# Optimization experiments

Measured on AMD Instinct MI355X. Metric: run time of the kernel, lower is better.

Reference implementation:

```python
import jax, jax.numpy as jnp
import numpy as np

B, T_ENC, T_DEC = 64, 512, 400
IN_DIM, R = 80, 2
D_ENC, D_ATT, D_PRE = 256, 256, 128
NEG_INF = -1e9


def _gru(x, h, Wi, Wh, bi, bh):
    # PyTorch GRUCell math
    gi = x @ Wi + bi
    gh = h @ Wh + bh
    ir, iz, inn = jnp.split(gi, 3, axis=-1)
    hr, hz, hn = jnp.split(gh, 3, axis=-1)
    r = jax.nn.sigmoid(ir + hr)
    z = jax.nn.sigmoid(iz + hz)
    n = jnp.tanh(inn + r * hn)
    return (1.0 - z) * n + z * h


def setup_inputs() -> dict:
    key = jax.random.key(0)
    ks = jax.random.split(key, 32)
    s = 0.05
    d_in = IN_DIM * R
    inp = {
        "encoder_outputs": jax.random.normal(ks[0], (B, T_ENC, D_ENC), jnp.float32),
        "inputs": jax.random.normal(ks[1], (B, T_DEC, d_in), jnp.float32),
        "memory_lengths": jax.random.randint(ks[2], (B,), T_ENC // 2, T_ENC + 1).astype(jnp.int32),
        # prenet
        "pre_W1": s * jax.random.normal(ks[3], (d_in, 256), jnp.float32),
        "pre_b1": jnp.zeros((256,), jnp.float32),
        "pre_W2": s * jax.random.normal(ks[4], (256, 128), jnp.float32),
        "pre_b2": jnp.zeros((128,), jnp.float32),
        # Bahdanau attention
        "mem_W": s * jax.random.normal(ks[5], (D_ENC, D_ATT), jnp.float32),
        "q_W": s * jax.random.normal(ks[6], (256, D_ATT), jnp.float32),
        "v_W": s * jax.random.normal(ks[7], (D_ATT, 1), jnp.float32),
        # attention GRUCell: input = cat(prenet 128, attention 256) = 384
        "att_Wi": s * jax.random.normal(ks[8], (384, 768), jnp.float32),
        "att_Wh": s * jax.random.normal(ks[9], (256, 768), jnp.float32),
        "att_bi": jnp.zeros((768,), jnp.float32),
        "att_bh": jnp.zeros((768,), jnp.float32),
        # project_to_decoder_in
        "proj_in_W": s * jax.random.normal(ks[10], (512, 256), jnp.float32),
        "proj_in_b": jnp.zeros((256,), jnp.float32),
        # decoder GRUCells
        "dec1_Wi": s * jax.random.normal(ks[11], (256, 768), jnp.float32),
        "dec1_Wh": s * jax.random.normal(ks[12], (256, 768), jnp.float32),
        "dec1_bi": jnp.zeros((768,), jnp.float32),
        "dec1_bh": jnp.zeros((768,), jnp.float32),
        "dec2_Wi": s * jax.random.normal(ks[13], (256, 768), jnp.float32),
        "dec2_Wh": s * jax.random.normal(ks[14], (256, 768), jnp.float32),
        "dec2_bi": jnp.zeros((768,), jnp.float32),
        "dec2_bh": jnp.zeros((768,), jnp.float32),
        # output projections
        "mel_W": s * jax.random.normal(ks[15], (256, d_in), jnp.float32),
        "mel_b": jnp.zeros((d_in,), jnp.float32),
        "gate_W": s * jax.random.normal(ks[16], (256, R), jnp.float32),
        "gate_b": jnp.zeros((R,), jnp.float32),
    }
    return inp


def _decoder_forward(encoder_outputs, inputs, memory_lengths,
                     pre_W1, pre_b1, pre_W2, pre_b2,
                     mem_W, q_W, v_W,
                     att_Wi, att_Wh, att_bi, att_bh,
                     proj_in_W, proj_in_b,
                     dec1_Wi, dec1_Wh, dec1_bi, dec1_bh,
                     dec2_Wi, dec2_Wh, dec2_bi, dec2_bh,
                     mel_W, mel_b, gate_W, gate_b):
    Bq, Tq, _ = encoder_outputs.shape
    processed_memory = encoder_outputs @ mem_W  # (B, T_enc, D_att)
    valid = jnp.arange(Tq)[None, :] < memory_lengths[:, None]  # (B, T_enc)

    # teacher forcing: input at step t is inputs[t-1], zeros at t=0
    prev = jnp.concatenate([jnp.zeros_like(inputs[:, :1]), inputs[:, :-1]], axis=1)
    prev = jnp.swapaxes(prev, 0, 1)  # (T_dec, B, in_dim*r)

    def prenet(x):
        # dropout is identity in eval mode
        h = jax.nn.relu(x @ pre_W1 + pre_b1)
        return jax.nn.relu(h @ pre_W2 + pre_b2)

    def step(carry, x_prev):
        att_h, h1, h2, cur_att = carry
        pre = prenet(x_prev)  # (B, 128)
        cell_in = jnp.concatenate([pre, cur_att], axis=-1)  # (B, 384)
        att_h = _gru(cell_in, att_h, att_Wi, att_Wh, att_bi, att_bh)  # (B, 256)
        # Bahdanau alignment over encoder memory
        score = jnp.squeeze(
            jnp.tanh(processed_memory + (att_h @ q_W)[:, None, :]) @ v_W, -1)  # (B, T_enc)
        score = jnp.where(valid, score, NEG_INF)
        align = jax.nn.softmax(score, axis=-1)
        cur_att = jnp.einsum('bt,btd->bd', align, encoder_outputs)  # (B, 256)
        dec_in = jnp.concatenate([att_h, cur_att], axis=-1) @ proj_in_W + proj_in_b
        h1 = _gru(dec_in, h1, dec1_Wi, dec1_Wh, dec1_bi, dec1_bh)
        d = h1 + dec_in
        h2 = _gru(d, h2, dec2_Wi, dec2_Wh, dec2_bi, dec2_bh)
        d = h2 + d
        gate = jax.nn.sigmoid(d @ gate_W + gate_b)  # (B, r)
        out = d @ mel_W + mel_b  # (B, in_dim*r)
        return (att_h, h1, h2, cur_att), (out, align, gate)

    z = jnp.zeros((Bq, 256), encoder_outputs.dtype)
    init = (z, z, z, z)
    _, (outs, aligns, gates) = jax.lax.scan(step, init, prev)
    outputs = jnp.swapaxes(outs, 0, 1)      # (B, T_dec, in_dim*r)
    alignments = jnp.swapaxes(aligns, 0, 1)  # (B, T_dec, T_enc)
    gates = jnp.swapaxes(gates, 0, 1)        # (B, T_dec, r)
    return outputs, alignments, gates


def reference(encoder_outputs, inputs, memory_lengths,
              pre_W1, pre_b1, pre_W2, pre_b2,
              mem_W, q_W, v_W,
              att_Wi, att_Wh, att_bi, att_bh,
              proj_in_W, proj_in_b,
              dec1_Wi, dec1_Wh, dec1_bi, dec1_bh,
              dec2_Wi, dec2_Wh, dec2_bi, dec2_bh,
              mel_W, mel_b, gate_W, gate_b):
    return _decoder_forward(encoder_outputs, inputs, memory_lengths,
                            pre_W1, pre_b1, pre_W2, pre_b2,
                            mem_W, q_W, v_W,
                            att_Wi, att_Wh, att_bi, att_bh,
                            proj_in_W, proj_in_b,
                            dec1_Wi, dec1_Wh, dec1_bi, dec1_bh,
                            dec2_Wi, dec2_Wh, dec2_bi, dec2_bh,
                            mel_W, mel_b, gate_W, gate_b)
```

## Files before the change

### kernel.cpp

```cpp
#include <hip/hip_runtime.h>

#define TDEC 400
#define NTH 512
#define NWG 256

typedef float f32x4 __attribute__((ext_vector_type(4)));
typedef unsigned u32x4 __attribute__((ext_vector_type(4)));
typedef unsigned u32x2 __attribute__((ext_vector_type(2)));

#define OFF_BAR   0
#define OFF_ATTH  11264
#define OFF_H1    44032
#define OFF_H2    76800
#define OFF_CURP  109568
#define OFF_ATTS  125952
#define OFF_Q     126208
#define ZERO_FLOATS 142592
#define OFF_D1    142592
#define OFF_SUMS  158976
#define OFF_C1    184576
#define OFF_PRE   185600
#define OFF_PMB   1824000
#define OFF_ENCB  6018304
#define OFF_D2A   10212608
#define T_WIT_A   10212608
#define T_WHT_A   10507520
#define T_M1T     10704128
#define T_WHT1    11097344
#define T_PJT     11293952
#define T_WIT2    11425024
#define T_WHT2    11621632
#define T_QWT     11818240
#define T_M1      11883776
#define OFF_BLOB  16766208

#define BLOB_N   26112
#define BLOB_STR 26624
#define BO_AI  0
#define BO_AH  4608
#define BO_Q   7680
#define BO_M1  8704
#define BO_H1  14848
#define BO_PJ  17920
#define BO_I2  19968
#define BO_H2  23040

#define AOFF 4096000
#define GOFF 17203200

#define MSTI  (8*1024)
#define GENI  (9*1024)
#define FAILI (10*1024)

__device__ __forceinline__ float fsig(float x){ return 1.0f/(1.0f+__expf(-x)); }
__device__ __forceinline__ float ftanh(float x){ float e = __expf(2.0f*x); return 1.0f - 2.0f/(e+1.0f); }
__device__ __forceinline__ float blo(unsigned u){ return __uint_as_float(u<<16); }
__device__ __forceinline__ float bhi(unsigned u){ return __uint_as_float(u & 0xffff0000u); }

__device__ __forceinline__ f32x4 cload16(const float* p){
  f32x4 r;
  asm volatile("global_load_dwordx4 %0, %1, off sc0 sc1" : "=v"(r) : "v"(p));
  return r;
}
__device__ __forceinline__ f32x4 cload16w(const float* p){
  f32x4 r;
  asm volatile("global_load_dwordx4 %0, %1, off sc0 sc1\n\ts_waitcnt vmcnt(0)" : "=v"(r) : "v"(p));
  return r;
}
__device__ __forceinline__ u32x4 cload16u(const unsigned short* p){
  u32x4 r;
  asm volatile("global_load_dwordx4 %0, %1, off sc0 sc1" : "=v"(r) : "v"(p));
  return r;
}
__device__ __forceinline__ float aload4(const float* p){
  unsigned u = __hip_atomic_load((const unsigned*)p, __ATOMIC_RELAXED, __HIP_MEMORY_SCOPE_AGENT);
  return __uint_as_float(u);
}
__device__ __forceinline__ void astore4(float* p, float v){
  __hip_atomic_store((unsigned*)p, __float_as_uint(v), __ATOMIC_RELAXED, __HIP_MEMORY_SCOPE_AGENT);
}
__device__ __forceinline__ void aadd(float* p, float v){
  __hip_atomic_fetch_add(p, v, __ATOMIC_RELAXED, __HIP_MEMORY_SCOPE_AGENT);
}
__device__ __forceinline__ int aloadi(const int* p){
  return __hip_atomic_load(p, __ATOMIC_RELAXED, __HIP_MEMORY_SCOPE_AGENT);
}

__device__ __forceinline__ void ldsbar(){
  __builtin_amdgcn_sched_barrier(0);
  asm volatile("s_waitcnt lgkmcnt(0)" ::: "memory");
  __builtin_amdgcn_s_barrier();
  __builtin_amdgcn_sched_barrier(0);
}

__device__ __forceinline__ void gbar(int* bar, int g, int l, int n){
  asm volatile("s_waitcnt vmcnt(0)" ::: "memory");
  __syncthreads();
  if (threadIdx.x == 0){
    if (aloadi(&bar[FAILI]) == 0){
      int a = __hip_atomic_fetch_add(&bar[(l&7)*1024 + g*64], 1, __ATOMIC_RELAXED, __HIP_MEMORY_SCOPE_AGENT);
      if (a == 8*n - 1){
        int m = __hip_atomic_fetch_add(&bar[MSTI + g*64], 1, __ATOMIC_RELAXED, __HIP_MEMORY_SCOPE_AGENT);
        if (m == 8*n - 1)
          __hip_atomic_store(&bar[GENI + g*64], n, __ATOMIC_RELAXED, __HIP_MEMORY_SCOPE_AGENT);
      }
      int sp = 0;
      while (aloadi(&bar[GENI + g*64]) < n){
        __builtin_amdgcn_s_sleep(1);
        if (++sp > (1<<20)){
          __hip_atomic_store(&bar[FAILI], 1, __ATOMIC_RELAXED, __HIP_MEMORY_SCOPE_AGENT);
          break;
        }
      }
    }
  }
  __syncthreads();
}

__device__ __forceinline__ unsigned short f2bf(float f){
  unsigned u = __float_as_uint(f);
  return (unsigned short)((u + 0x7fffu + ((u>>16)&1u)) >> 16);
}

template<int N8>
__device__ __forceinline__ float bdot(const unsigned short* wr, const float* xr){
  f32x4 accA = 0.f, accB = 0.f;
  #pragma unroll 4
  for (int k = 0; k < N8; ++k){
    u32x4 u = *(const u32x4*)(wr + k*8);
    f32x4 a = *(const f32x4*)(xr + k*8);
    f32x4 b = *(const f32x4*)(xr + k*8 + 4);
    f32x4 w0, w1;
    w0[0]=blo(u[0]); w0[1]=bhi(u[0]); w0[2]=blo(u[1]); w0[3]=bhi(u[1]);
    w1[0]=blo(u[2]); w1[1]=bhi(u[2]); w1[2]=blo(u[3]); w1[3]=bhi(u[3]);
    accA += w0*a; accB += w1*b;
  }
  f32x4 s = accA + accB;
  return s[0]+s[1]+s[2]+s[3];
}

__global__ __launch_bounds__(256, 1) void transpose_k(const float* __restrict__ in,
                                                      float* __restrict__ outp, int K, int C){
  __shared__ float tl[32][33];
  int c0 = blockIdx.x * 32, k0 = blockIdx.y * 32;
  int tx = threadIdx.x & 31, ty = threadIdx.x >> 5;
  for (int i = ty; i < 32; i += 8){
    int k = k0 + i, c = c0 + tx;
    if (k < K && c < C) tl[i][tx] = in[k * C + c];
  }
  __syncthreads();
  for (int i = ty; i < 32; i += 8){
    int c = c0 + i, k = k0 + tx;
    if (c < C && k < K) outp[c * K + k] = tl[tx][i];
  }
}

__global__ __launch_bounds__(128, 1) void fuse_k(const float* __restrict__ projW,
    const float* __restrict__ d1Wi, float* __restrict__ M1){
  int jt = blockIdx.x % 6, i = blockIdx.x / 6;
  int j = jt * 128 + threadIdx.x;
  float acc = 0.f;
  for (int k = 0; k < 256; ++k) acc += projW[i*256+k] * d1Wi[k*768+j];
  M1[i*768+j] = acc;
}

__global__ __launch_bounds__(256, 1) void c1_k(const float* __restrict__ projB,
    const float* __restrict__ d1Wi, const float* __restrict__ d1Bi, float* __restrict__ C1){
  int j = blockIdx.x * 256 + threadIdx.x;
  float acc = d1Bi[j];
  for (int k = 0; k < 256; ++k) acc += projB[k] * d1Wi[k*768+j];
  C1[j] = acc;
}

__global__ __launch_bounds__(512, 1) void pack_k(float* __restrict__ ws){
  int sl = blockIdx.x;
  const float* TAI = ws + T_WIT_A;
  const float* TAH = ws + T_WHT_A;
  const float* TM1 = ws + T_M1T;
  const float* TH1 = ws + T_WHT1;
  const float* TPJ = ws + T_PJT;
  const float* TI2 = ws + T_WIT2;
  const float* TH2 = ws + T_WHT2;
  const float* TQ  = ws + T_QWT;
  unsigned short* blob = (unsigned short*)(ws + OFF_BLOB) + (size_t)sl * BLOB_STR;
  for (int idx = threadIdx.x; idx < BLOB_N; idx += 512){
    float v; int cs, k, o;
    if (idx < BO_AH){ cs = idx / 384; k = idx - cs*384;
      v = TAI[((cs%3)*256 + sl*4 + cs/3)*384 + k]; }
    else if (idx < BO_Q){ o = idx - BO_AH; cs = o >> 8; k = o & 255;
      v = TAH[((cs%3)*256 + sl*4 + cs/3)*256 + k]; }
    else if (idx < BO_M1){ o = idx - BO_Q; cs = o >> 8; k = o & 255;
      v = TQ[(sl*4 + cs)*256 + k]; }
    else if (idx < BO_H1){ o = idx - BO_M1; cs = o >> 9; k = o & 511;
      v = TM1[((cs%3)*256 + sl*4 + cs/3)*512 + k]; }
    else if (idx < BO_PJ){ o = idx - BO_H1; cs = o >> 8; k = o & 255;
      v = TH1[((cs%3)*256 + sl*4 + cs/3)*256 + k]; }
    else if (idx < BO_I2){ o = idx - BO_PJ; cs = o >> 9; k = o & 511;
      v = TPJ[(sl*4 + cs)*512 + k]; }
    else if (idx < BO_H2){ o = idx - BO_I2; cs = o >> 8; k = o & 255;
      v = TI2[((cs%3)*256 + sl*4 + cs/3)*256 + k]; }
    else { o = idx - BO_H2; cs = o >> 8; k = o & 255;
      v = TH2[((cs%3)*256 + sl*4 + cs/3)*256 + k]; }
    blob[idx] = f2bf(v);
  }
}

__global__ __launch_bounds__(256, 1) void qt_k(const float* __restrict__ ws,
                                               float* __restrict__ out){
  unsigned short* qtb = (unsigned short*)(out + GOFF);
  const float* TQ = ws + T_QWT;
  int idx = blockIdx.x * 256 + threadIdx.x;
  int it = idx >> 11, j = (idx >> 3) & 255, e = idx & 7;
  qtb[idx] = f2bf(TQ[j*256 + it*8 + e]);
}

__global__ __launch_bounds__(NTH, 1) void prenet_k(float* __restrict__ ws,
    const float* __restrict__ inp, const float* __restrict__ W1, const float* __restrict__ B1,
    const float* __restrict__ W2, const float* __restrict__ B2){
  __shared__ float xT[160 * 33];
  __shared__ float hT[256 * 33];
  int t = blockIdx.x, half = blockIdx.y, tid = threadIdx.x;
  int bbase = half * 32;
  for (int r = tid; r < 32 * 160; r += NTH){
    int b2 = r / 160; int k = r - b2 * 160;
    xT[k * 33 + b2] = (t == 0) ? 0.f : inp[((bbase + b2) * TDEC + (t - 1)) * 160 + k];
  }
  __syncthreads();
  int bl = tid & 31, slot = tid >> 5;
  float acc1[16];
  #pragma unroll
  for (int i = 0; i < 16; ++i) acc1[i] = 0.f;
  for (int k = 0; k < 160; ++k){
    float xv = xT[k * 33 + bl];
    const float* wr = W1 + k * 256 + slot * 16;
    #pragma unroll
    for (int i = 0; i < 16; ++i) acc1[i] += xv * wr[i];
  }
  #pragma unroll
  for (int i = 0; i < 16; ++i){
    int c = slot * 16 + i;
    hT[c * 33 + bl] = fmaxf(acc1[i] + B1[c], 0.f);
  }
  __syncthreads();
  float acc2[8];
  #pragma unroll
  for (int i = 0; i < 8; ++i) acc2[i] = 0.f;
  for (int k = 0; k < 256; ++k){
    float hv = hT[k * 33 + bl];
    const float* wr = W2 + k * 128 + slot * 8;
    #pragma unroll
    for (int i = 0; i < 8; ++i) acc2[i] += hv * wr[i];
  }
  unsigned short* dst = (unsigned short*)(ws + OFF_PRE) + (size_t)t*8192 + (bbase + bl)*128 + slot*8;
  u32x4 pk;
  #pragma unroll
  for (int i = 0; i < 4; ++i){
    float v0 = fmaxf(acc2[2*i] + B2[slot*8 + 2*i], 0.f);
    float v1 = fmaxf(acc2[2*i+1] + B2[slot*8 + 2*i+1], 0.f);
    pk[i] = (unsigned)f2bf(v0) | ((unsigned)f2bf(v1) << 16);
  }
  *(u32x4*)dst = pk;
}

__global__ __launch_bounds__(NTH, 1) void pm_k(float* __restrict__ ws,
    const float* __restrict__ enc, const float* __restrict__ memW){
  int wg = blockIdx.x, tid = threadIdx.x;
  int b = wg & 63, th = wg >> 6;
  int slot = tid & 7, tt = tid >> 3;
  int trow = th * 64 + tt;
  const float* er = enc + ((size_t)(b * 512 + trow)) * 256;
  f32x4 acc[8];
  #pragma unroll
  for (int i = 0; i < 8; ++i) acc[i] = 0.f;
  for (int k = 0; k < 256; ++k){
    float ev = er[k];
    const f32x4* wr = (const f32x4*)(memW + k * 256 + slot * 32);
    #pragma unroll
    for (int i = 0; i < 8; ++i) acc[i] += ev * wr[i];
  }
  unsigned short* pmB = (unsigned short*)(ws + OFF_PMB);
  unsigned short* dst = pmB + ((size_t)(b * 512 + trow)) * 256 + slot * 32;
  #pragma unroll
  for (int i = 0; i < 8; ++i){
    u32x2 pk;
    pk[0] = (unsigned)f2bf(acc[i][0]) | ((unsigned)f2bf(acc[i][1]) << 16);
    pk[1] = (unsigned)f2bf(acc[i][2]) | ((unsigned)f2bf(acc[i][3]) << 16);
    *(u32x2*)(dst + i * 4) = pk;
  }
  const float* e2 = enc + ((size_t)(b * 512 + th * 64)) * 256;
  unsigned* eb = (unsigned*)((unsigned short*)(ws + OFF_ENCB) + ((size_t)(b * 512 + th * 64)) * 256);
  for (int i = tid; i < 64 * 128; i += NTH){
    float v0 = e2[i * 2], v1 = e2[i * 2 + 1];
    eb[i] = (unsigned)f2bf(v0) | ((unsigned)f2bf(v1) << 16);
  }
}

__global__ __launch_bounds__(NTH, 2) void decoder_k(
    float* __restrict__ ws, float* __restrict__ out,
    const int* __restrict__ memlen,
    const float* __restrict__ vW,
    const float* __restrict__ attBi, const float* __restrict__ attBh,
    const float* __restrict__ projB,
    const float* __restrict__ d1Bh,
    const float* __restrict__ d2Bi, const float* __restrict__ d2Bh)
{
  const int wg = blockIdx.x, tid = threadIdx.x;
  int* bar = (int*)ws;
  float* attH = ws + OFF_ATTH;
  float* h1a  = ws + OFF_H1;
  float* h2a  = ws + OFF_H2;
  float* const curB[2]  = { ws + OFF_CURP, ws + OFF_Q };
  float* const attSB[2] = { ws + OFF_ATTS, ws + OFF_ATTS + 64 };
  float* d1v  = ws + OFF_D1;
  const float* C1v = ws + OFF_C1;
  const unsigned short* preB16 = (const unsigned short*)(ws + OFF_PRE);
  const unsigned short* pmB  = (const unsigned short*)(ws + OFF_PMB);
  const unsigned short* encB = (const unsigned short*)(ws + OFF_ENCB);
  const unsigned short* qtb = (const unsigned short*)(out + GOFF);
  float* d2a  = ws + OFF_D2A;

  __shared__ float BUF[12416];
  __shared__ float qL[256], vL[256];
  __shared__ float eL[128];
  __shared__ float ewGi[192], ewGh[192], pdec[128];

  if (tid < 256) vL[tid] = vW[tid];

  const int g = wg >> 6, l = wg & 63;
  const int sl = l;
  const int b0 = g << 4;
  const int b2 = b0 + (l >> 2), ch2 = l & 3;
  const int len2 = memlen[b2];
  const unsigned short* blob = (const unsigned short*)(ws + OFF_BLOB) + (size_t)sl * BLOB_STR;

  const int bq = tid & 15, x = tid >> 4;
  const int cs = (x >= 12) ? (x - 12) : x;
  const int gg = cs % 3, jh = cs / 3;
  const int col = gg * 256 + sl * 4 + jh;

  const int r0 = tid >> 6, c0 = (tid & 63) << 2;
  const int r1 = r0 + 8;
  const int prr = tid >> 4, pcc = (tid & 15) * 8;

  u32x4 pmv[8], env[8];
  {
    int te = tid >> 2, part = tid & 3;
    const u32x4* pmp = (const u32x4*)(pmB + ((size_t)(b2*512 + ch2*128 + te))*256 + part*64);
    #pragma unroll
    for (int i = 0; i < 8; ++i) pmv[i] = pmp[i];
    int ich = tid >> 5, dblk = tid & 31;
    const unsigned short* ep = encB + ((size_t)(b2*512 + ch2*128 + ich*8))*256 + dblk*8;
    #pragma unroll
    for (int i = 0; i < 8; ++i) env[i] = *(const u32x4*)(ep + i*256);
  }

  f32x4 pH0, pH1, pC0, pC1;
  float pS0, pS1;
  u32x4 ppre = 0u;
  {
    const float* gHn = attH + 16384 + b0*256;
    const float* gCn = curB[1] + b0*256;
    pH0 = cload16(gHn + (r0<<8) + c0); pH1 = cload16(gHn + (r1<<8) + c0);
    pC0 = cload16(gCn + (r0<<8) + c0); pC1 = cload16(gCn + (r1<<8) + c0);
    pS0 = aload4(attSB[1] + b0 + r0);  pS1 = aload4(attSB[1] + b0 + r1);
    if (tid < 256) ppre = cload16u(preB16 + (b0 + prr)*128 + pcc);
  }

  int bn = 0;
  for (int t = 0; t < TDEC; ++t){
    const int w = t & 1, rb = w ^ 1;
    f32x4 eA0, eA1, eH0, eH1, eG0, eG1;

    {
      float* xL = BUF;
      float* hL = BUF + 6208;
      asm volatile("s_waitcnt vmcnt(0)" : "+v"(pH0),"+v"(pH1),"+v"(pC0),"+v"(pC1),"+v"(ppre));
      float iv0 = pS0 > 0.f ? 1.f/pS0 : 0.f, iv1 = pS1 > 0.f ? 1.f/pS1 : 0.f;
      if (tid < 256){
        float* xd = xL + prr*388 + pcc;
        xd[0]=blo(ppre[0]); xd[1]=bhi(ppre[0]); xd[2]=blo(ppre[1]); xd[3]=bhi(ppre[1]);
        xd[4]=blo(ppre[2]); xd[5]=bhi(ppre[2]); xd[6]=blo(ppre[3]); xd[7]=bhi(ppre[3]);
      }
      *(f32x4*)(hL + r0*260 + c0) = pH0; *(f32x4*)(hL + r1*260 + c0) = pH1;
      *(f32x4*)(xL + r0*388 + 128 + c0) = pC0*iv0; *(f32x4*)(xL + r1*388 + 128 + c0) = pC1*iv1;
      if (tid < 64) astore4(curB[w] + wg*64 + tid, 0.f);
      if (sl == 0 && tid < 16) astore4(attSB[w] + b0 + tid, 0.f);
      ldsbar();
      if (x < 12)
        ewGi[cs*16 + bq] = bdot<48>(blob + BO_AI + cs*384, xL + bq*388) + attBi[col];
      else if (x < 24)
        ewGh[cs*16 + bq] = bdot<32>(blob + BO_AH + cs*256, hL + bq*260) + attBh[col];
      ldsbar();
      if (tid < 64){
        int bt = tid & 15, jj = tid >> 4;
        int j = sl*4 + jj;
        float ir = ewGi[(jj*3+0)*16+bt] + ewGh[(jj*3+0)*16+bt];
        float iz = ewGi[(jj*3+1)*16+bt] + ewGh[(jj*3+1)*16+bt];
        float inn = ewGi[(jj*3+2)*16+bt];
        float hn  = ewGh[(jj*3+2)*16+bt];
        float rg = fsig(ir), z = fsig(iz);
        float n = ftanh(inn + rg * hn);
        float h = hL[bt*260 + j];
        astore4(attH + w*16384 + (b0+bt)*256 + j, (1.f - z)*n + z*h);
      }
    }
    gbar(bar, g, l, ++bn);

    {
      float* ctxP = BUF;
      float* qIn  = BUF + 8192;
      eA0 = cload16(attH + w*16384 + ((b0+r0)<<8) + c0);
      eA1 = cload16(attH + w*16384 + ((b0+r1)<<8) + c0);
      eH0 = cload16(h1a + rb*16384 + ((b0+r0)<<8) + c0);
      eH1 = cload16(h1a + rb*16384 + ((b0+r1)<<8) + c0);
      eG0 = cload16(h2a + rb*16384 + ((b0+r0)<<8) + c0);
      eG1 = cload16(h2a + rb*16384 + ((b0+r1)<<8) + c0);
      if (tid < 64){
        f32x4 v = cload16w(attH + w*16384 + b2*256 + tid*4);
        *(f32x4*)(qIn + tid*4) = v;
      }
      ldsbar();
      {
        int lane = tid & 63;
        int j = (tid >> 6)*32 + (lane & 31), hf = lane >> 5;
        const unsigned short* qw = qtb + j*8 + (size_t)hf*32768;
        const float* qx = qIn + hf*128;
        f32x4 aA = 0.f, aB = 0.f;
        #pragma unroll 4
        for (int it = 0; it < 16; ++it){
          u32x4 u = *(const u32x4*)(qw + (size_t)it*2048);
          f32x4 a = *(const f32x4*)(qx + it*8);
          f32x4 b = *(const f32x4*)(qx + it*8 + 4);
          f32x4 w0, w1;
          w0[0]=blo(u[0]); w0[1]=bhi(u[0]); w0[2]=blo(u[1]); w0[3]=bhi(u[1]);
          w1[0]=blo(u[2]); w1[1]=bhi(u[2]); w1[2]=blo(u[3]); w1[3]=bhi(u[3]);
          aA += w0*a; aB += w1*b;
        }
        f32x4 s4 = aA + aB;
        float s = s4[0]+s4[1]+s4[2]+s4[3];
        s += __shfl_xor(s, 32);
        if (hf == 0) qL[j] = s;
      }
      ldsbar();
      {
        int te = tid >> 2, part = tid & 3;
        int ge = ch2*128 + te;
        float a4 = 0.f;
        #pragma unroll
        for (int i = 0; i < 8; ++i){
          u32x4 u = pmv[i];
          int kb = part*64 + i*8;
          a4 += ftanh(blo(u[0]) + qL[kb+0]) * vL[kb+0];
          a4 += ftanh(bhi(u[0]) + qL[kb+1]) * vL[kb+1];
          a4 += ftanh(blo(u[1]) + qL[kb+2]) * vL[kb+2];
          a4 += ftanh(bhi(u[1]) + qL[kb+3]) * vL[kb+3];
          a4 += ftanh(blo(u[2]) + qL[kb+4]) * vL[kb+4];
          a4 += ftanh(bhi(u[2]) + qL[kb+5]) * vL[kb+5];
          a4 += ftanh(blo(u[3]) + qL[kb+6]) * vL[kb+6];
          a4 += ftanh(bhi(u[3]) + qL[kb+7]) * vL[kb+7];
        }
        a4 += __shfl_xor(a4, 1);
        a4 += __shfl_xor(a4, 2);
        float e = (ge < len2) ? __expf(a4) : 0.f;
        if (part == 0){
          eL[te] = e;
          out[AOFF + ((size_t)(b2*TDEC + t))*512 + ge] = e;
        }
      }
      ldsbar();
      if (tid < 64){
        float s = eL[tid] + eL[tid + 64];
        #pragma unroll
        for (int o = 32; o > 0; o >>= 1) s += __shfl_down(s, o);
        if (tid == 0) aadd(attSB[w] + b2, s);
      }
      {
        int ich = tid >> 5, dblk = tid & 31;
        f32x4 acA = 0.f, acB = 0.f;
        #pragma unroll
        for (int i = 0; i < 8; ++i){
          u32x4 u = env[i];
          float e = eL[ich*8 + i];
          acA[0] += e*blo(u[0]); acA[1] += e*bhi(u[0]);
          acA[2] += e*blo(u[1]); acA[3] += e*bhi(u[1]);
          acB[0] += e*blo(u[2]); acB[1] += e*bhi(u[2]);
          acB[2] += e*blo(u[3]); acB[3] += e*bhi(u[3]);
        }
        *(f32x4*)(ctxP + tid*8) = acA;
        *(f32x4*)(ctxP + tid*8 + 4) = acB;
      }
      ldsbar();
      if (tid < 256){
        int dblk = tid >> 3, d = tid & 7;
        float s = 0.f;
        #pragma unroll
        for (int i = 0; i < 16; ++i) s += ctxP[i*256 + dblk*8 + d];
        aadd(curB[w] + b2*256 + dblk*8 + d, s);
      }
    }
    gbar(bar, g, l, ++bn);

    {
      float* yL  = BUF;
      float* h1L = BUF + 8256;
      const float* gC = curB[w] + b0*256;
      f32x4 vC0 = cload16(gC + (r0<<8) + c0), vC1 = cload16(gC + (r1<<8) + c0);
      float s0 = aload4(attSB[w] + b0 + r0), s1 = aload4(attSB[w] + b0 + r1);
      asm volatile("s_waitcnt vmcnt(0)" : "+v"(eA0),"+v"(eA1),"+v"(eH0),"+v"(eH1),"+v"(vC0),"+v"(vC1));
      float iv0 = s0 > 0.f ? 1.f/s0 : 0.f, iv1 = s1 > 0.f ? 1.f/s1 : 0.f;
      *(f32x4*)(yL + r0*516 + c0) = eA0;       *(f32x4*)(yL + r1*516 + c0) = eA1;
      *(f32x4*)(h1L + r0*260 + c0) = eH0;      *(f32x4*)(h1L + r1*260 + c0) = eH1;
      *(f32x4*)(yL + r0*516 + 256 + c0) = vC0*iv0; *(f32x4*)(yL + r1*516 + 256 + c0) = vC1*iv1;
      ldsbar();
      if (x < 12)
        ewGi[cs*16 + bq] = bdot<64>(blob + BO_M1 + cs*512, yL + bq*516) + C1v[col];
      else if (x < 24)
        ewGh[cs*16 + bq] = bdot<32>(blob + BO_H1 + cs*256, h1L + bq*260) + d1Bh[col];
      else {
        int idx = tid - 384;
        int bq2 = idx & 15, cc = (idx >> 4) & 3, half = idx >> 6;
        pdec[idx] = bdot<32>(blob + BO_PJ + cc*512 + half*256, yL + bq2*516 + half*256);
      }
      ldsbar();
      if (tid < 64){
        int bt = tid & 15, jj = tid >> 4;
        int j = sl*4 + jj;
        float ir = ewGi[(jj*3+0)*16+bt] + ewGh[(jj*3+0)*16+bt];
        float iz = ewGi[(jj*3+1)*16+bt] + ewGh[(jj*3+1)*16+bt];
        float inn = ewGi[(jj*3+2)*16+bt];
        float hn  = ewGh[(jj*3+2)*16+bt];
        float rg = fsig(ir), z = fsig(iz);
        float n = ftanh(inn + rg * hn);
        float hv = h1L[bt*260 + j];
        float hnew = (1.f - z)*n + z*hv;
        float dec = pdec[jj*16 + bt] + pdec[64 + jj*16 + bt] + projB[j];
        astore4(h1a + w*16384 + (b0+bt)*256 + j, hnew);
        astore4(d1v + (b0+bt)*256 + j, hnew + dec);
      }
      if (sl == 0 && tid < 16)
        ws[OFF_SUMS + t*64 + b0 + tid] = aload4(attSB[w] + b0 + tid);
    }
    gbar(bar, g, l, ++bn);

    {
      float* dL  = BUF;
      float* h2L = BUF + 4160;
      const float* gD = d1v + b0*256;
      f32x4 vD0 = cload16(gD + (r0<<8) + c0), vD1 = cload16(gD + (r1<<8) + c0);
      asm volatile("s_waitcnt vmcnt(0)" : "+v"(vD0),"+v"(vD1),"+v"(eG0),"+v"(eG1));
      {
        const float* gHn = attH + w*16384 + b0*256;
        const float* gCn = curB[w] + b0*256;
        pH0 = cload16(gHn + (r0<<8) + c0); pH1 = cload16(gHn + (r1<<8) + c0);
        pC0 = cload16(gCn + (r0<<8) + c0); pC1 = cload16(gCn + (r1<<8) + c0);
        pS0 = aload4(attSB[w] + b0 + r0);  pS1 = aload4(attSB[w] + b0 + r1);
        int tn = (t + 1 < TDEC) ? (t + 1) : 0;
        if (tid < 256) ppre = cload16u(preB16 + (size_t)tn*8192 + (b0 + prr)*128 + pcc);
      }
      *(f32x4*)(dL + r0*260 + c0) = vD0;  *(f32x4*)(dL + r1*260 + c0) = vD1;
      *(f32x4*)(h2L + r0*260 + c0) = eG0; *(f32x4*)(h2L + r1*260 + c0) = eG1;
      ldsbar();
      if (x < 12)
        ewGi[cs*16 + bq] = bdot<32>(blob + BO_I2 + cs*256, dL + bq*260) + d2Bi[col];
      else if (x < 24)
        ewGh[cs*16 + bq] = bdot<32>(blob + BO_H2 + cs*256, h2L + bq*260) + d2Bh[col];
      ldsbar();
      if (tid < 64){
        int bt = tid & 15, jj = tid >> 4;
        int j = sl*4 + jj;
        float ir = ewGi[(jj*3+0)*16+bt] + ewGh[(jj*3+0)*16+bt];
        float iz = ewGi[(jj*3+1)*16+bt] + ewGh[(jj*3+1)*16+bt];
        float inn = ewGi[(jj*3+2)*16+bt];
        float hn  = ewGh[(jj*3+2)*16+bt];
        float rg = fsig(ir), z = fsig(iz);
        float n = ftanh(inn + rg * hn);
        float hv = h2L[bt*260 + j];
        float hnew = (1.f - z)*n + z*hv;
        astore4(h2a + w*16384 + (b0+bt)*256 + j, hnew);
        d2a[t*16384 + j*64 + (b0+bt)] = hnew + dL[bt*260 + j];
      }
      ldsbar();
    }
  }
}

__global__ __launch_bounds__(NTH, 1) void rescale_k(const float* __restrict__ ws,
                                                    float* __restrict__ out){
  int blk = blockIdx.x;
  int b = blk / TDEC, t = blk - b * TDEC;
  float s = ws[OFF_SUMS + t*64 + b];
  float inv = (s > 0.f) ? 1.f/s : 0.f;
  out[AOFF + (size_t)blk*512 + threadIdx.x] *= inv;
}

__global__ __launch_bounds__(NTH, 1) void outproj_k(const float* __restrict__ ws,
    float* __restrict__ out, const float* __restrict__ melW, const float* __restrict__ melB,
    const float* __restrict__ gateW, const float* __restrict__ gateB){
  int t = blockIdx.x, tid = threadIdx.x;
  int cx = tid & 255, bh = tid >> 8;
  const float* src = ws + OFF_D2A + t*16384 + bh*32;
  float acc[32];
  #pragma unroll
  for (int i = 0; i < 32; ++i) acc[i] = 0.f;
  bool ismel = (cx < 160);
  bool isgate = (cx >= 160 && cx < 162);
  for (int j = 0; j < 256; ++j){
    float wv = 0.f;
    if (ismel) wv = melW[j*160 + cx];
    else if (isgate) wv = gateW[j*2 + (cx - 160)];
    const f32x4* dp = (const f32x4*)(src + j*64);
    f32x4 vv[8];
    #pragma unroll
    for (int q = 0; q < 8; ++q) vv[q] = dp[q];
    #pragma unroll
    for (int q = 0; q < 8; ++q){
      acc[q*4+0] += vv[q][0]*wv; acc[q*4+1] += vv[q][1]*wv;
      acc[q*4+2] += vv[q][2]*wv; acc[q*4+3] += vv[q][3]*wv;
    }
  }
  if (ismel){
    float bb = melB[cx];
    #pragma unroll
    for (int i = 0; i < 32; ++i){
      int b = bh*32 + i;
      out[((size_t)(b*TDEC + t))*160 + cx] = acc[i] + bb;
    }
  } else if (isgate){
    int g = cx - 160;
    float bb = gateB[g];
    #pragma unroll
    for (int i = 0; i < 32; ++i){
      int b = bh*32 + i;
      out[GOFF + ((size_t)(b*TDEC + t))*2 + g] = fsig(acc[i] + bb);
    }
  }
}

extern "C" void kernel_launch(void* const* d_in, const int* in_sizes, int n_in,
                              void* d_out, int out_size, void* d_ws, size_t ws_size,
                              hipStream_t stream)
{
  (void)in_sizes; (void)n_in; (void)out_size; (void)ws_size;
  const float* enc   = (const float*)d_in[0];
  const float* inp   = (const float*)d_in[1];
  const int*   mlen  = (const int*)d_in[2];
  const float* preW1 = (const float*)d_in[3];
  const float* preB1 = (const float*)d_in[4];
  const float* preW2 = (const float*)d_in[5];
  const float* preB2 = (const float*)d_in[6];
  const float* memW  = (const float*)d_in[7];
  const float* qW    = (const float*)d_in[8];
  const float* vW    = (const float*)d_in[9];
  const float* attWi = (const float*)d_in[10];
  const float* attWh = (const float*)d_in[11];
  const float* attBi = (const float*)d_in[12];
  const float* attBh = (const float*)d_in[13];
  const float* projW = (const float*)d_in[14];
  const float* projB = (const float*)d_in[15];
  const float* d1Wi  = (const float*)d_in[16];
  const float* d1Wh  = (const float*)d_in[17];
  const float* d1Bi  = (const float*)d_in[18];
  const float* d1Bh  = (const float*)d_in[19];
  const float* d2Wi  = (const float*)d_in[20];
  const float* d2Wh  = (const float*)d_in[21];
  const float* d2Bi  = (const float*)d_in[22];
  const float* d2Bh  = (const float*)d_in[23];
  const float* melW  = (const float*)d_in[24];
  const float* melB  = (const float*)d_in[25];
  const float* gateW = (const float*)d_in[26];
  const float* gateB = (const float*)d_in[27];
  float* ws = (float*)d_ws;
  float* out = (float*)d_out;

  hipMemsetAsync(d_ws, 0, (size_t)ZERO_FLOATS * sizeof(float), stream);

  dim3 tt(256);
  transpose_k<<<dim3(24, 12), tt, 0, stream>>>(attWi, ws + T_WIT_A, 384, 768);
  transpose_k<<<dim3(24, 8),  tt, 0, stream>>>(attWh, ws + T_WHT_A, 256, 768);
  transpose_k<<<dim3(24, 8),  tt, 0, stream>>>(d1Wh,  ws + T_WHT1, 256, 768);
  transpose_k<<<dim3(24, 8),  tt, 0, stream>>>(d2Wi,  ws + T_WIT2, 256, 768);
  transpose_k<<<dim3(24, 8),  tt, 0, stream>>>(d2Wh,  ws + T_WHT2, 256, 768);
  transpose_k<<<dim3(8, 16),  tt, 0, stream>>>(projW, ws + T_PJT, 512, 256);
  transpose_k<<<dim3(8, 8),   tt, 0, stream>>>(qW,    ws + T_QWT, 256, 256);
  fuse_k<<<3072, 128, 0, stream>>>(projW, d1Wi, ws + T_M1);
  c1_k<<<3, 256, 0, stream>>>(projB, d1Wi, d1Bi, ws + OFF_C1);
  transpose_k<<<dim3(24, 16), tt, 0, stream>>>(ws + T_M1, ws + T_M1T, 512, 768);
  pack_k<<<64, NTH, 0, stream>>>(ws);
  qt_k<<<256, 256, 0, stream>>>(ws, out);

  prenet_k<<<dim3(TDEC, 2), NTH, 0, stream>>>(ws, inp, preW1, preB1, preW2, preB2);
  pm_k<<<512, NTH, 0, stream>>>(ws, enc, memW);
  decoder_k<<<NWG, NTH, 0, stream>>>(ws, out, mlen, vW, attBi, attBh, projB,
                                     d1Bh, d2Bi, d2Bh);
  rescale_k<<<64 * TDEC, NTH, 0, stream>>>(ws, out);
  outproj_k<<<TDEC, NTH, 0, stream>>>(ws, out, melW, melB, gateW, gateB);
}
```

Measured before the change: 13.21 ms.

## Skew decoder phases across timesteps to halve grid barriers per step

Restructures the persistent recurrent kernel's per-timestep schedule. The old loop ran four phases separated by four grid-wide barriers; the new loop software-pipelines them so the attention GRU for step t+1 runs alongside decoder GRU1 for step t, and decoder GRU2 for step t-1 runs alongside the attention query/energy phase. That leaves two grid barriers per iteration, with prologue and epilogue iterations gated by flags. It also hoists bias loads into registers and replaces the separate shared-memory arrays with one shared pool. The trade is more work and more shared-memory traffic between barriers, plus more complex step-index bookkeeping.

```diff
diff --git a/kernel.cpp b/kernel.cpp
--- a/kernel.cpp
+++ b/kernel.cpp
@@ -60,11 +60,6 @@
 __device__ __forceinline__ f32x4 cload16(const float* p){
   f32x4 r;
   asm volatile("global_load_dwordx4 %0, %1, off sc0 sc1" : "=v"(r) : "v"(p));
-  return r;
-}
-__device__ __forceinline__ f32x4 cload16w(const float* p){
-  f32x4 r;
-  asm volatile("global_load_dwordx4 %0, %1, off sc0 sc1\n\ts_waitcnt vmcnt(0)" : "=v"(r) : "v"(p));
   return r;
 }
 __device__ __forceinline__ u32x4 cload16u(const unsigned short* p){
@@ -319,10 +314,23 @@
   const unsigned short* qtb = (const unsigned short*)(out + GOFF);
   float* d2a  = ws + OFF_D2A;
 
-  __shared__ float BUF[12416];
-  __shared__ float qL[256], vL[256];
-  __shared__ float eL[128];
-  __shared__ float ewGi[192], ewGh[192], pdec[128];
+  __shared__ float POOL[16128];
+  float* const ahL  = POOL;
+  float* const cnL  = POOL + 4160;
+  float* const h1L  = POOL + 8320;
+  float* const xpre = POOL + 12480;
+  float* const dL   = POOL;
+  float* const h2L  = POOL + 4160;
+  float* const ctxP = POOL + 8320;
+  float* const qIn  = POOL + 12416;
+  float* const ewGi  = POOL + 14592;
+  float* const ewGh  = POOL + 14784;
+  float* const ewGi2 = POOL + 14976;
+  float* const ewGh2 = POOL + 15168;
+  float* const pdec  = POOL + 15360;
+  float* const qL    = POOL + 15488;
+  float* const vL    = POOL + 15744;
+  float* const eL    = POOL + 16000;
 
   if (tid < 256) vL[tid] = vW[tid];
 
@@ -334,13 +342,19 @@
   const unsigned short* blob = (const unsigned short*)(ws + OFF_BLOB) + (size_t)sl * BLOB_STR;
 
   const int bq = tid & 15, x = tid >> 4;
-  const int cs = (x >= 12) ? (x - 12) : x;
+  const int cs = (x >= 12 && x < 24) ? (x - 12) : x;
   const int gg = cs % 3, jh = cs / 3;
   const int col = gg * 256 + sl * 4 + jh;
 
   const int r0 = tid >> 6, c0 = (tid & 63) << 2;
   const int r1 = r0 + 8;
   const int prr = tid >> 4, pcc = (tid & 15) * 8;
+
+  float rb0 = 0.f, rb1 = 0.f, rb2 = 0.f;
+  if (x < 12){ rb0 = attBi[col]; rb1 = C1v[col];  rb2 = d2Bi[col]; }
+  else if (x < 24){ rb0 = attBh[col]; rb1 = d1Bh[col]; rb2 = d2Bh[col]; }
+  float pjB2 = 0.f;
+  if (tid >= 64 && tid < 128) pjB2 = projB[sl*4 + ((tid - 64) >> 4)];
 
   u32x4 pmv[8], env[8];
   {
@@ -354,73 +368,41 @@
     for (int i = 0; i < 8; ++i) env[i] = *(const u32x4*)(ep + i*256);
   }
 
-  f32x4 pH0, pH1, pC0, pC1;
-  float pS0, pS1;
+  f32x4 eA0, eA1, eH0, eH1;
   u32x4 ppre = 0u;
-  {
-    const float* gHn = attH + 16384 + b0*256;
-    const float* gCn = curB[1] + b0*256;
-    pH0 = cload16(gHn + (r0<<8) + c0); pH1 = cload16(gHn + (r1<<8) + c0);
-    pC0 = cload16(gCn + (r0<<8) + c0); pC1 = cload16(gCn + (r1<<8) + c0);
-    pS0 = aload4(attSB[1] + b0 + r0);  pS1 = aload4(attSB[1] + b0 + r1);
-    if (tid < 256) ppre = cload16u(preB16 + (b0 + prr)*128 + pcc);
-  }
+  eA0 = cload16(attH + 16384 + ((b0+r0)<<8) + c0);
+  eA1 = cload16(attH + 16384 + ((b0+r1)<<8) + c0);
+  eH0 = cload16(h1a + ((b0+r0)<<8) + c0);
+  eH1 = cload16(h1a + ((b0+r1)<<8) + c0);
+  if (tid < 256) ppre = cload16u(preB16 + (b0 + prr)*128 + pcc);
 
   int bn = 0;
-  for (int t = 0; t < TDEC; ++t){
-    const int w = t & 1, rb = w ^ 1;
-    f32x4 eA0, eA1, eH0, eH1, eG0, eG1;
-
-    {
-      float* xL = BUF;
-      float* hL = BUF + 6208;
-      asm volatile("s_waitcnt vmcnt(0)" : "+v"(pH0),"+v"(pH1),"+v"(pC0),"+v"(pC1),"+v"(ppre));
-      float iv0 = pS0 > 0.f ? 1.f/pS0 : 0.f, iv1 = pS1 > 0.f ? 1.f/pS1 : 0.f;
-      if (tid < 256){
-        float* xd = xL + prr*388 + pcc;
-        xd[0]=blo(ppre[0]); xd[1]=bhi(ppre[0]); xd[2]=blo(ppre[1]); xd[3]=bhi(ppre[1]);
-        xd[4]=blo(ppre[2]); xd[5]=bhi(ppre[2]); xd[6]=blo(ppre[3]); xd[7]=bhi(ppre[3]);
-      }
-      *(f32x4*)(hL + r0*260 + c0) = pH0; *(f32x4*)(hL + r1*260 + c0) = pH1;
-      *(f32x4*)(xL + r0*388 + 128 + c0) = pC0*iv0; *(f32x4*)(xL + r1*388 + 128 + c0) = pC1*iv1;
-      if (tid < 64) astore4(curB[w] + wg*64 + tid, 0.f);
-      if (sl == 0 && tid < 16) astore4(attSB[w] + b0 + tid, 0.f);
-      ldsbar();
-      if (x < 12)
-        ewGi[cs*16 + bq] = bdot<48>(blob + BO_AI + cs*384, xL + bq*388) + attBi[col];
-      else if (x < 24)
-        ewGh[cs*16 + bq] = bdot<32>(blob + BO_AH + cs*256, hL + bq*260) + attBh[col];
-      ldsbar();
-      if (tid < 64){
-        int bt = tid & 15, jj = tid >> 4;
-        int j = sl*4 + jj;
-        float ir = ewGi[(jj*3+0)*16+bt] + ewGh[(jj*3+0)*16+bt];
-        float iz = ewGi[(jj*3+1)*16+bt] + ewGh[(jj*3+1)*16+bt];
-        float inn = ewGi[(jj*3+2)*16+bt];
-        float hn  = ewGh[(jj*3+2)*16+bt];
-        float rg = fsig(ir), z = fsig(iz);
-        float n = ftanh(inn + rg * hn);
-        float h = hL[bt*260 + j];
-        astore4(attH + w*16384 + (b0+bt)*256 + j, (1.f - z)*n + z*h);
-      }
-    }
-    gbar(bar, g, l, ++bn);
-
-    {
-      float* ctxP = BUF;
-      float* qIn  = BUF + 8192;
+  for (int t = -1; t <= 400; ++t){
+    const int w = t & 1, wn = w ^ 1;
+
+    if (t >= 0){
+      const bool doP2 = (t < 400), doP5 = (t >= 1);
+      f32x4 vD0 = cload16(d1v + ((b0+r0)<<8) + c0);
+      f32x4 vD1 = cload16(d1v + ((b0+r1)<<8) + c0);
+      f32x4 vH0 = cload16(h2a + w*16384 + ((b0+r0)<<8) + c0);
+      f32x4 vH1 = cload16(h2a + w*16384 + ((b0+r1)<<8) + c0);
+      f32x4 qv = 0.f;
+      if (tid < 64) qv = cload16(attH + w*16384 + b2*256 + tid*4);
       eA0 = cload16(attH + w*16384 + ((b0+r0)<<8) + c0);
       eA1 = cload16(attH + w*16384 + ((b0+r1)<<8) + c0);
-      eH0 = cload16(h1a + rb*16384 + ((b0+r0)<<8) + c0);
-      eH1 = cload16(h1a + rb*16384 + ((b0+r1)<<8) + c0);
-      eG0 = cload16(h2a + rb*16384 + ((b0+r0)<<8) + c0);
-      eG1 = cload16(h2a + rb*16384 + ((b0+r1)<<8) + c0);
-      if (tid < 64){
-        f32x4 v = cload16w(attH + w*16384 + b2*256 + tid*4);
-        *(f32x4*)(qIn + tid*4) = v;
-      }
+      eH0 = cload16(h1a + wn*16384 + ((b0+r0)<<8) + c0);
+      eH1 = cload16(h1a + wn*16384 + ((b0+r1)<<8) + c0);
+      {
+        int tn = (t + 1 < TDEC) ? (t + 1) : (TDEC - 1);
+        if (tid < 256) ppre = cload16u(preB16 + (size_t)tn*8192 + (b0 + prr)*128 + pcc);
+      }
+      asm volatile("s_waitcnt vmcnt(0)" : "+v"(vD0),"+v"(vD1),"+v"(vH0),"+v"(vH1),"+v"(qv));
+      __builtin_amdgcn_sched_barrier(0);
+      if (tid < 64) *(f32x4*)(qIn + tid*4) = qv;
+      *(f32x4*)(dL + r0*260 + c0) = vD0;  *(f32x4*)(dL + r1*260 + c0) = vD1;
+      *(f32x4*)(h2L + r0*260 + c0) = vH0; *(f32x4*)(h2L + r1*260 + c0) = vH1;
       ldsbar();
-      {
+      if (doP2){
         int lane = tid & 63;
         int j = (tid >> 6)*32 + (lane & 31), hf = lane >> 5;
         const unsigned short* qw = qtb + j*8 + (size_t)hf*32768;
@@ -441,8 +423,14 @@
         s += __shfl_xor(s, 32);
         if (hf == 0) qL[j] = s;
       }
+      if (doP5){
+        if (x < 12)
+          ewGi[cs*16 + bq] = bdot<32>(blob + BO_I2 + cs*256, dL + bq*260) + rb2;
+        else if (x < 24)
+          ewGh[cs*16 + bq] = bdot<32>(blob + BO_H2 + cs*256, h2L + bq*260) + rb2;
+      }
       ldsbar();
-      {
+      if (doP2){
         int te = tid >> 2, part = tid & 3;
         int ge = ch2*128 + te;
         float a4 = 0.f;
@@ -467,105 +455,7 @@
           out[AOFF + ((size_t)(b2*TDEC + t))*512 + ge] = e;
         }
       }
-      ldsbar();
-      if (tid < 64){
-        float s = eL[tid] + eL[tid + 64];
-        #pragma unroll
-        for (int o = 32; o > 0; o >>= 1) s += __shfl_down(s, o);
-        if (tid == 0) aadd(attSB[w] + b2, s);
-      }
-      {
-        int ich = tid >> 5, dblk = tid & 31;
-        f32x4 acA = 0.f, acB = 0.f;
-        #pragma unroll
-        for (int i = 0; i < 8; ++i){
-          u32x4 u = env[i];
-          float e = eL[ich*8 + i];
-          acA[0] += e*blo(u[0]); acA[1] += e*bhi(u[0]);
-          acA[2] += e*blo(u[1]); acA[3] += e*bhi(u[1]);
-          acB[0] += e*blo(u[2]); acB[1] += e*bhi(u[2]);
-          acB[2] += e*blo(u[3]); acB[3] += e*bhi(u[3]);
-        }
-        *(f32x4*)(ctxP + tid*8) = acA;
-        *(f32x4*)(ctxP + tid*8 + 4) = acB;
-      }
-      ldsbar();
-      if (tid < 256){
-        int dblk = tid >> 3, d = tid & 7;
-        float s = 0.f;
-        #pragma unroll
-        for (int i = 0; i < 16; ++i) s += ctxP[i*256 + dblk*8 + d];
-        aadd(curB[w] + b2*256 + dblk*8 + d, s);
-      }
-    }
-    gbar(bar, g, l, ++bn);
-
-    {
-      float* yL  = BUF;
-      float* h1L = BUF + 8256;
-      const float* gC = curB[w] + b0*256;
-      f32x4 vC0 = cload16(gC + (r0<<8) + c0), vC1 = cload16(gC + (r1<<8) + c0);
-      float s0 = aload4(attSB[w] + b0 + r0), s1 = aload4(attSB[w] + b0 + r1);
-      asm volatile("s_waitcnt vmcnt(0)" : "+v"(eA0),"+v"(eA1),"+v"(eH0),"+v"(eH1),"+v"(vC0),"+v"(vC1));
-      float iv0 = s0 > 0.f ? 1.f/s0 : 0.f, iv1 = s1 > 0.f ? 1.f/s1 : 0.f;
-      *(f32x4*)(yL + r0*516 + c0) = eA0;       *(f32x4*)(yL + r1*516 + c0) = eA1;
-      *(f32x4*)(h1L + r0*260 + c0) = eH0;      *(f32x4*)(h1L + r1*260 + c0) = eH1;
-      *(f32x4*)(yL + r0*516 + 256 + c0) = vC0*iv0; *(f32x4*)(yL + r1*516 + 256 + c0) = vC1*iv1;
-      ldsbar();
-      if (x < 12)
-        ewGi[cs*16 + bq] = bdot<64>(blob + BO_M1 + cs*512, yL + bq*516) + C1v[col];
-      else if (x < 24)
-        ewGh[cs*16 + bq] = bdot<32>(blob + BO_H1 + cs*256, h1L + bq*260) + d1Bh[col];
-      else {
-        int idx = tid - 384;
-        int bq2 = idx & 15, cc = (idx >> 4) & 3, half = idx >> 6;
-        pdec[idx] = bdot<32>(blob + BO_PJ + cc*512 + half*256, yL + bq2*516 + half*256);
-      }
-      ldsbar();
-      if (tid < 64){
-        int bt = tid & 15, jj = tid >> 4;
-        int j = sl*4 + jj;
-        float ir = ewGi[(jj*3+0)*16+bt] + ewGh[(jj*3+0)*16+bt];
-        float iz = ewGi[(jj*3+1)*16+bt] + ewGh[(jj*3+1)*16+bt];
-        float inn = ewGi[(jj*3+2)*16+bt];
-        float hn  = ewGh[(jj*3+2)*16+bt];
-        float rg = fsig(ir), z = fsig(iz);
-        float n = ftanh(inn + rg * hn);
-        float hv = h1L[bt*260 + j];
-        float hnew = (1.f - z)*n + z*hv;
-        float dec = pdec[jj*16 + bt] + pdec[64 + jj*16 + bt] + projB[j];
-        astore4(h1a + w*16384 + (b0+bt)*256 + j, hnew);
-        astore4(d1v + (b0+bt)*256 + j, hnew + dec);
-      }
-      if (sl == 0 && tid < 16)
-        ws[OFF_SUMS + t*64 + b0 + tid] = aload4(attSB[w] + b0 + tid);
-    }
-    gbar(bar, g, l, ++bn);
-
-    {
-      float* dL  = BUF;
-      float* h2L = BUF + 4160;
-      const float* gD = d1v + b0*256;
-      f32x4 vD0 = cload16(gD + (r0<<8) + c0), vD1 = cload16(gD + (r1<<8) + c0);
-      asm volatile("s_waitcnt vmcnt(0)" : "+v"(vD0),"+v"(vD1),"+v"(eG0),"+v"(eG1));
-      {
-        const float* gHn = attH + w*16384 + b0*256;
-        const float* gCn = curB[w] + b0*256;
-        pH0 = cload16(gHn + (r0<<8) + c0); pH1 = cload16(gHn + (r1<<8) + c0);
-        pC0 = cload16(gCn + (r0<<8) + c0); pC1 = cload16(gCn + (r1<<8) + c0);
-        pS0 = aload4(attSB[w] + b0 + r0);  pS1 = aload4(attSB[w] + b0 + r1);
-        int tn = (t + 1 < TDEC) ? (t + 1) : 0;
-        if (tid < 256) ppre = cload16u(preB16 + (size_t)tn*8192 + (b0 + prr)*128 + pcc);
-      }
-      *(f32x4*)(dL + r0*260 + c0) = vD0;  *(f32x4*)(dL + r1*260 + c0) = vD1;
-      *(f32x4*)(h2L + r0*260 + c0) = eG0; *(f32x4*)(h2L + r1*260 + c0) = eG1;
-      ldsbar();
-      if (x < 12)
-        ewGi[cs*16 + bq] = bdot<32>(blob + BO_I2 + cs*256, dL + bq*260) + d2Bi[col];
-      else if (x < 24)
-        ewGh[cs*16 + bq] = bdot<32>(blob + BO_H2 + cs*256, h2L + bq*260) + d2Bh[col];
-      ldsbar();
-      if (tid < 64){
+      if (doP5 && tid < 64){
         int bt = tid & 15, jj = tid >> 4;
         int j = sl*4 + jj;
         float ir = ewGi[(jj*3+0)*16+bt] + ewGh[(jj*3+0)*16+bt];
@@ -576,11 +466,115 @@
         float n = ftanh(inn + rg * hn);
         float hv = h2L[bt*260 + j];
         float hnew = (1.f - z)*n + z*hv;
-        astore4(h2a + w*16384 + (b0+bt)*256 + j, hnew);
-        d2a[t*16384 + j*64 + (b0+bt)] = hnew + dL[bt*260 + j];
+        astore4(h2a + wn*16384 + (b0+bt)*256 + j, hnew);
+        d2a[(size_t)(t-1)*16384 + j*64 + (b0+bt)] = hnew + dL[bt*260 + j];
       }
       ldsbar();
+      if (doP2){
+        if (tid < 64){
+          float s = eL[tid] + eL[tid + 64];
+          #pragma unroll
+          for (int o = 32; o > 0; o >>= 1) s += __shfl_down(s, o);
+          if (tid == 0) aadd(attSB[w] + b2, s);
+        }
+        {
+          int ich = tid >> 5, dblk = tid & 31;
+          f32x4 acA = 0.f, acB = 0.f;
+          #pragma unroll
+          for (int i = 0; i < 8; ++i){
+            u32x4 u = env[i];
+            float e = eL[ich*8 + i];
+            acA[0] += e*blo(u[0]); acA[1] += e*bhi(u[0]);
+            acA[2] += e*blo(u[1]); acA[3] += e*bhi(u[1]);
+            acB[0] += e*blo(u[2]); acB[1] += e*bhi(u[2]);
+            acB[2] += e*blo(u[3]); acB[3] += e*bhi(u[3]);
+          }
+          *(f32x4*)(ctxP + tid*8) = acA;
+          *(f32x4*)(ctxP + tid*8 + 4) = acB;
+        }
+      }
+      ldsbar();
+      if (doP2 && tid < 256){
+        int dblk = tid >> 3, d = tid & 7;
+        float s = 0.f;
+        #pragma unroll
+        for (int i = 0; i < 16; ++i) s += ctxP[i*256 + dblk*8 + d];
+        aadd(curB[w] + b2*256 + dblk*8 + d, s);
+      }
     }
+
+    gbar(bar, g, l, ++bn);
+    if (t == 400) break;
+
+    {
+      const bool doP0 = (t <= 398), doP4 = (t >= 0);
+      f32x4 vC0 = cload16(curB[w] + ((b0+r0)<<8) + c0);
+      f32x4 vC1 = cload16(curB[w] + ((b0+r1)<<8) + c0);
+      float s0 = aload4(attSB[w] + b0 + r0), s1 = aload4(attSB[w] + b0 + r1);
+      asm volatile("s_waitcnt vmcnt(0)" : "+v"(vC0),"+v"(vC1));
+      __builtin_amdgcn_sched_barrier(0);
+      float iv0 = s0 > 0.f ? 1.f/s0 : 0.f, iv1 = s1 > 0.f ? 1.f/s1 : 0.f;
+      *(f32x4*)(ahL + r0*260 + c0) = eA0; *(f32x4*)(ahL + r1*260 + c0) = eA1;
+      *(f32x4*)(h1L + r0*260 + c0) = eH0; *(f32x4*)(h1L + r1*260 + c0) = eH1;
+      *(f32x4*)(cnL + r0*260 + c0) = vC0*iv0; *(f32x4*)(cnL + r1*260 + c0) = vC1*iv1;
+      if (tid < 256){
+        float* xd = xpre + prr*132 + pcc;
+        xd[0]=blo(ppre[0]); xd[1]=bhi(ppre[0]); xd[2]=blo(ppre[1]); xd[3]=bhi(ppre[1]);
+        xd[4]=blo(ppre[2]); xd[5]=bhi(ppre[2]); xd[6]=blo(ppre[3]); xd[7]=bhi(ppre[3]);
+      }
+      if (tid < 64) astore4(curB[wn] + wg*64 + tid, 0.f);
+      if (sl == 0 && tid < 16) astore4(attSB[wn] + b0 + tid, 0.f);
+      if (t >= 0 && sl == 0 && tid < 16)
+        ws[OFF_SUMS + t*64 + b0 + tid] = aload4(attSB[w] + b0 + tid);
+      ldsbar();
+      if (x < 12){
+        if (doP0)
+          ewGi[cs*16 + bq] = bdot<16>(blob + BO_AI + cs*384, xpre + bq*132)
+                           + bdot<32>(blob + BO_AI + cs*384 + 128, cnL + bq*260) + rb0;
+        if (doP4)
+          ewGi2[cs*16 + bq] = bdot<32>(blob + BO_M1 + cs*512, ahL + bq*260)
+                            + bdot<32>(blob + BO_M1 + cs*512 + 256, cnL + bq*260) + rb1;
+      } else if (x < 24){
+        if (doP0)
+          ewGh[cs*16 + bq] = bdot<32>(blob + BO_AH + cs*256, ahL + bq*260) + rb0;
+        if (doP4)
+          ewGh2[cs*16 + bq] = bdot<32>(blob + BO_H1 + cs*256, h1L + bq*260) + rb1;
+      } else if (doP4){
+        int idx = tid - 384;
+        int bq2 = idx & 15, cc = (idx >> 4) & 3, half = idx >> 6;
+        pdec[idx] = bdot<32>(blob + BO_PJ + cc*512 + half*256, (half ? cnL : ahL) + bq2*260);
+      }
+      ldsbar();
+      if (doP0 && tid < 64){
+        int bt = tid & 15, jj = tid >> 4;
+        int j = sl*4 + jj;
+        float ir = ewGi[(jj*3+0)*16+bt] + ewGh[(jj*3+0)*16+bt];
+        float iz = ewGi[(jj*3+1)*16+bt] + ewGh[(jj*3+1)*16+bt];
+        float inn = ewGi[(jj*3+2)*16+bt];
+        float hn  = ewGh[(jj*3+2)*16+bt];
+        float rg = fsig(ir), z = fsig(iz);
+        float n = ftanh(inn + rg * hn);
+        float h = ahL[bt*260 + j];
+        astore4(attH + wn*16384 + (b0+bt)*256 + j, (1.f - z)*n + z*h);
+      }
+      if (doP4 && tid >= 64 && tid < 128){
+        int t2 = tid - 64;
+        int bt = t2 & 15, jj = t2 >> 4;
+        int j = sl*4 + jj;
+        float ir = ewGi2[(jj*3+0)*16+bt] + ewGh2[(jj*3+0)*16+bt];
+        float iz = ewGi2[(jj*3+1)*16+bt] + ewGh2[(jj*3+1)*16+bt];
+        float inn = ewGi2[(jj*3+2)*16+bt];
+        float hn  = ewGh2[(jj*3+2)*16+bt];
+        float rg = fsig(ir), z = fsig(iz);
+        float n = ftanh(inn + rg * hn);
+        float hv = h1L[bt*260 + j];
+        float hnew = (1.f - z)*n + z*hv;
+        float dec = pdec[jj*16 + bt] + pdec[64 + jj*16 + bt] + pjB2;
+        astore4(h1a + w*16384 + (b0+bt)*256 + j, hnew);
+        astore4(d1v + (b0+bt)*256 + j, hnew + dec);
+      }
+    }
+    gbar(bar, g, l, ++bn);
   }
 }
 
```

New measurement: 12.02 ms. 9.0% less time.
